# Optimization experiments

Hardware: AMD Instinct MI355X
Metric: run time of the kernel (lower is better)

The kernel has to match this reference:

```python
import jax, jax.numpy as jnp
import numpy as np

H = 16
D_MODEL = 1024
D_K = D_MODEL // H


def setup_inputs() -> dict:
    key = jax.random.key(0)
    ks = jax.random.split(key, 11)
    B, S = 4, 2048
    scale = 1.0 / np.sqrt(D_MODEL)
    inp = {
        "query": jax.random.normal(ks[0], (B, S, D_MODEL), dtype=jnp.float32),
        "key": jax.random.normal(ks[1], (B, S, D_MODEL), dtype=jnp.float32),
        "value": jax.random.normal(ks[2], (B, S, D_MODEL), dtype=jnp.float32),
        "Wq": jax.random.normal(ks[3], (D_MODEL, D_MODEL), dtype=jnp.float32) * scale,
        "bq": jnp.zeros((D_MODEL,), dtype=jnp.float32),
        "Wk": jax.random.normal(ks[4], (D_MODEL, D_MODEL), dtype=jnp.float32) * scale,
        "bk": jnp.zeros((D_MODEL,), dtype=jnp.float32),
        "Wv": jax.random.normal(ks[5], (D_MODEL, D_MODEL), dtype=jnp.float32) * scale,
        "bv": jnp.zeros((D_MODEL,), dtype=jnp.float32),
        "Wo": jax.random.normal(ks[6], (D_MODEL, D_MODEL), dtype=jnp.float32) * scale,
        "bo": jnp.zeros((D_MODEL,), dtype=jnp.float32),
    }
    return inp


def reference(query, key, value, Wq, bq, Wk, bk, Wv, bv, Wo, bo):
    B, S, _ = query.shape

    def proj(x, W, b):
        # nn.Linear: x @ W.T + b, then split heads -> [B, H, S, D_K]
        y = jnp.einsum("bsd,ed->bse", x, W) + b
        return y.reshape(B, S, H, D_K).transpose(0, 2, 1, 3)

    q = proj(query, Wq, bq)
    k = proj(key, Wk, bk)
    v = proj(value, Wv, bv)

    scores = jnp.einsum("bhqd,bhkd->bhqk", q, k) / jnp.sqrt(jnp.float32(D_K))
    attn = jax.nn.softmax(scores, axis=-1)
    out = jnp.einsum("bhqk,bhkd->bhqd", attn, v)  # [B,H,S,D_K]
    out = out.transpose(0, 2, 1, 3).reshape(B, S, H * D_K)
    # final linear (dropout disabled in eval / deterministic reference)
    return jnp.einsum("bsd,ed->bse", out, Wo) + bo
```

## Files before the change

### kernel.cpp

```cpp
#include <hip/hip_runtime.h>
#include <stdint.h>

typedef __attribute__((ext_vector_type(8))) short short8;
typedef __attribute__((ext_vector_type(4))) float floatx4;

#define DEV __device__ __forceinline__

DEV unsigned short f2bf(float x) {
  unsigned u = __float_as_uint(x);
  u += 0x7fffu + ((u >> 16) & 1u);
  return (unsigned short)(u >> 16);
}

DEV unsigned pkbf(float hi, float lo) {
  return __builtin_amdgcn_perm(__float_as_uint(hi) + 0x8000u,
                               __float_as_uint(lo) + 0x8000u, 0x07060302u);
}

DEV unsigned cvtpk(float a, float b) {
  unsigned r;
  asm("v_cvt_pk_bf16_f32 %0, %1, %2" : "=v"(r) : "v"(a), "v"(b));
  return r;
}

DEV void load_lds16(const unsigned short* g, unsigned short* l) {
  __builtin_amdgcn_global_load_lds(
      (const __attribute__((address_space(1))) void*)g,
      (__attribute__((address_space(3))) void*)l, 16, 0, 0);
}

DEV void lds_fence() { asm volatile("" ::: "memory"); }

#define ASM_VMCNT(n) asm volatile("s_waitcnt vmcnt(" #n ")" ::: "memory")
DEV void sched_fence() { __builtin_amdgcn_sched_barrier(0); }

__global__ void cvt_all(const float* __restrict__ Wq, const float* __restrict__ Wk,
                        const float* __restrict__ Wv, const float* __restrict__ Wo,
                        const float* __restrict__ Xq, const float* __restrict__ Xk,
                        const float* __restrict__ Xv,
                        unsigned short* __restrict__ Wb, unsigned short* __restrict__ XqB,
                        unsigned short* __restrict__ XkB, unsigned short* __restrict__ XvB) {
  int bid = blockIdx.x;
  const float* src;
  unsigned short* dst;
  int off;
  if (bid < 4096) {
    int sel = bid >> 10;
    src = sel == 0 ? Wq : sel == 1 ? Wk : sel == 2 ? Wv : Wo;
    dst = Wb + (size_t)sel * 1048576;
    off = bid & 1023;
  } else {
    bid -= 4096;
    int sel = bid >> 13;
    src = sel == 0 ? Xq : sel == 1 ? Xk : Xv;
    dst = sel == 0 ? XqB : sel == 1 ? XkB : XvB;
    off = bid & 8191;
  }
  int i = (off * 256 + threadIdx.x) * 4;
  float4 v = *(const float4*)(src + i);
  uint2 o;
  o.x = pkbf(v.y, v.x);
  o.y = pkbf(v.w, v.z);
  *(uint2*)(dst + i) = o;
}

#define SCQ (0.125f * 1.44269504089f)
__global__ __launch_bounds__(256, 3) void qkv_gemm(
    const unsigned short* __restrict__ XqB, const unsigned short* __restrict__ XkB,
    const unsigned short* __restrict__ XvB,
    const unsigned short* __restrict__ Wb,
    const float* __restrict__ bq, const float* __restrict__ bk, const float* __restrict__ bv,
    unsigned short* __restrict__ Qp, unsigned short* __restrict__ Kp,
    unsigned short* __restrict__ VTp) {
  __shared__ alignas(16) unsigned short Xs[3][128 * 32];
  __shared__ alignas(16) unsigned short Ws[3][128 * 32];
  const int z = blockIdx.z;
  const unsigned short* X = z == 0 ? XqB : z == 1 ? XkB : XvB;
  const unsigned short* W = Wb + (size_t)z * 1048576;
  const float* bias = z == 0 ? bq : z == 1 ? bk : bv;

  const int tid = threadIdx.x;
  const int lane = tid & 63, wave = tid >> 6;
  const int lcol = lane & 15, quad = lane >> 4;
  const int n2 = blockIdx.x + 8 * blockIdx.y;
  const int xcd = n2 & 7, ii = n2 >> 3;
  const int wo = (ii >> 3) * 128;
  const int xo = (xcd * 8 + (ii & 7)) * 128;
  const int wm = (wave & 1) * 64;
  const int wn = (wave >> 1) * 64;

  floatx4 acc[4][4];
  for (int mi = 0; mi < 4; ++mi)
    for (int ni = 0; ni < 4; ++ni)
      for (int r = 0; r < 4; ++r) acc[mi][ni][r] = 0.f;

  auto stage = [&](int kt, int buf) {
    const int k0 = kt * 32;
    int c = tid;
    load_lds16(W + (size_t)(wo + (c >> 2)) * 1024 + k0 + (c & 3) * 8, Ws[buf] + c * 8);
    load_lds16(X + (size_t)(xo + (c >> 2)) * 1024 + k0 + (c & 3) * 8, Xs[buf] + c * 8);
    c = tid + 256;
    load_lds16(W + (size_t)(wo + (c >> 2)) * 1024 + k0 + (c & 3) * 8, Ws[buf] + c * 8);
    load_lds16(X + (size_t)(xo + (c >> 2)) * 1024 + k0 + (c & 3) * 8, Xs[buf] + c * 8);
  };

  stage(0, 0);
  stage(1, 1);
  int cur = 0;
  for (int kt = 0; kt < 32; ++kt) {
    sched_fence();
    ASM_VMCNT(4);
    __builtin_amdgcn_s_barrier();
    sched_fence();
    int nb = cur + 2; if (nb >= 3) nb -= 3;
    stage((kt + 2) & 31, nb);
    const unsigned short* Ab = (z < 2) ? Ws[cur] : Xs[cur];
    const unsigned short* Bb = (z < 2) ? Xs[cur] : Ws[cur];
    short8 af[4], bfr[4];
#pragma unroll
    for (int mi = 0; mi < 4; ++mi)
      af[mi] = *(const short8*)(Ab + (wm + mi * 16 + lcol) * 32 + quad * 8);
#pragma unroll
    for (int ni = 0; ni < 4; ++ni)
      bfr[ni] = *(const short8*)(Bb + (wn + ni * 16 + lcol) * 32 + quad * 8);
#pragma unroll
    for (int mi = 0; mi < 4; ++mi)
#pragma unroll
      for (int ni = 0; ni < 4; ++ni)
        acc[mi][ni] = __builtin_amdgcn_mfma_f32_16x16x32_bf16(af[mi], bfr[ni], acc[mi][ni], 0, 0, 0);
    cur = (cur == 2) ? 0 : cur + 1;
  }

  if (z < 2) {
    unsigned short* Out = z == 0 ? Qp : Kp;
    const float scl = z == 0 ? SCQ : 1.f;
#pragma unroll
    for (int mi = 0; mi < 4; ++mi) {
      int dbase = wo + wm + mi * 16 + quad * 4;
      float4 bv4 = *(const float4*)(bias + dbase);
      int h = dbase >> 6, dk = dbase & 63;
#pragma unroll
      for (int ni = 0; ni < 4; ++ni) {
        int sg = xo + wn + ni * 16 + lcol;
        int bb = sg >> 11, ss = sg & 2047;
        uint2 o;
        o.x = pkbf((acc[mi][ni][1] + bv4.y) * scl, (acc[mi][ni][0] + bv4.x) * scl);
        o.y = pkbf((acc[mi][ni][3] + bv4.w) * scl, (acc[mi][ni][2] + bv4.z) * scl);
        *(uint2*)(Out + ((size_t)(bb * 16 + h) * 2048 + ss) * 64 + dk) = o;
      }
    }
  } else {
#pragma unroll
    for (int ni = 0; ni < 4; ++ni) {
      int dg = wo + wn + ni * 16 + lcol;
      float bvx = bias[dg];
      int h = dg >> 6, dk = dg & 63;
#pragma unroll
      for (int mi = 0; mi < 4; ++mi) {
        int sbase = xo + wm + mi * 16 + quad * 4;
        int bb = sbase >> 11, ss = sbase & 2047;
        uint2 o;
        o.x = pkbf(acc[mi][ni][1] + bvx, acc[mi][ni][0] + bvx);
        o.y = pkbf(acc[mi][ni][3] + bvx, acc[mi][ni][2] + bvx);
        *(uint2*)(VTp + ((size_t)(bb * 16 + h) * 64 + dk) * 2048 + ss) = o;
      }
    }
  }
}

__global__ __launch_bounds__(256, 3) void gemm_o(
    const unsigned short* __restrict__ A, const unsigned short* __restrict__ Bw,
    const float* __restrict__ bias, float* __restrict__ Out) {
  __shared__ alignas(16) unsigned short Cs[3][128 * 32];
  __shared__ alignas(16) unsigned short Wos[3][128 * 32];
  const int tid = threadIdx.x;
  const int lane = tid & 63, wave = tid >> 6;
  const int lcol = lane & 15, quad = lane >> 4;
  const int n2 = blockIdx.x + 8 * blockIdx.y;
  const int xcd = n2 & 7, ii = n2 >> 3;
  const int co = (ii >> 3) * 128;
  const int so = (xcd * 8 + (ii & 7)) * 128;
  const int wm = (wave & 1) * 64;
  const int wn = (wave >> 1) * 64;

  floatx4 acc[4][4];
  for (int mi = 0; mi < 4; ++mi)
    for (int ni = 0; ni < 4; ++ni)
      for (int r = 0; r < 4; ++r) acc[mi][ni][r] = 0.f;

  auto stage = [&](int kt, int buf) {
    const int k0 = kt * 32;
    int c = tid;
    load_lds16(Bw + (size_t)(co + (c >> 2)) * 1024 + k0 + (c & 3) * 8, Wos[buf] + c * 8);
    load_lds16(A  + (size_t)(so + (c >> 2)) * 1024 + k0 + (c & 3) * 8, Cs[buf] + c * 8);
    c = tid + 256;
    load_lds16(Bw + (size_t)(co + (c >> 2)) * 1024 + k0 + (c & 3) * 8, Wos[buf] + c * 8);
    load_lds16(A  + (size_t)(so + (c >> 2)) * 1024 + k0 + (c & 3) * 8, Cs[buf] + c * 8);
  };

  stage(0, 0);
  stage(1, 1);
  int cur = 0;
  for (int kt = 0; kt < 32; ++kt) {
    sched_fence();
    ASM_VMCNT(4);
    __builtin_amdgcn_s_barrier();
    sched_fence();
    int nb = cur + 2; if (nb >= 3) nb -= 3;
    stage((kt + 2) & 31, nb);
    short8 af[4], bfr[4];
#pragma unroll
    for (int mi = 0; mi < 4; ++mi)
      af[mi] = *(const short8*)(Wos[cur] + (wm + mi * 16 + lcol) * 32 + quad * 8);
#pragma unroll
    for (int ni = 0; ni < 4; ++ni)
      bfr[ni] = *(const short8*)(Cs[cur] + (wn + ni * 16 + lcol) * 32 + quad * 8);
#pragma unroll
    for (int mi = 0; mi < 4; ++mi)
#pragma unroll
      for (int ni = 0; ni < 4; ++ni)
        acc[mi][ni] = __builtin_amdgcn_mfma_f32_16x16x32_bf16(af[mi], bfr[ni], acc[mi][ni], 0, 0, 0);
    cur = (cur == 2) ? 0 : cur + 1;
  }
#pragma unroll
  for (int mi = 0; mi < 4; ++mi) {
    int cb = co + wm + mi * 16 + quad * 4;
    float4 bv4 = *(const float4*)(bias + cb);
#pragma unroll
    for (int ni = 0; ni < 4; ++ni) {
      int sg = so + wn + ni * 16 + lcol;
      float4 o;
      o.x = acc[mi][ni][0] + bv4.x;
      o.y = acc[mi][ni][1] + bv4.y;
      o.z = acc[mi][ni][2] + bv4.z;
      o.w = acc[mi][ni][3] + bv4.w;
      *(float4*)(Out + (size_t)sg * 1024 + cb) = o;
    }
  }
}

__global__ __launch_bounds__(256, 4) void attn_kernel(
    const unsigned short* __restrict__ Qp, const unsigned short* __restrict__ Kp,
    const unsigned short* __restrict__ VTp, unsigned short* __restrict__ Ctx) {
  __shared__ alignas(16) unsigned short Ks[2][64 * 64];
  __shared__ alignas(16) unsigned short Vt[64 * 64];
  __shared__ alignas(16) unsigned short Ps[128 * 64];

  const int tid = threadIdx.x;
  const int lane = tid & 63, wave = tid >> 6;
  const int lcol = lane & 15, quad = lane >> 4;
  const int wq = wave * 32;
  const int n = blockIdx.x + 16 * (blockIdx.y + 16 * blockIdx.z);
  const int xcd = n & 7, ii = n >> 3;
  const int hb = xcd * 8 + (ii & 7);
  const int qt = ii >> 3;
  const size_t bh = (size_t)hb * 2048 * 64;
  const int b = hb >> 4;
  const unsigned short* Qb = Qp + bh + (size_t)qt * 128 * 64;
  const unsigned short* Kb = Kp + bh;
  const unsigned short* VTb = VTp + bh;

#pragma unroll
  for (int i = 0; i < 4; ++i) {
    int p = tid + i * 256;
    int row = p >> 3, pj = p & 7;
    load_lds16(Qb + row * 64 + ((pj ^ (row & 7)) * 8), Ps + p * 8);
  }
#pragma unroll
  for (int i = 0; i < 2; ++i) {
    int p = tid + i * 256;
    int kr = p >> 3, kj = p & 7;
    load_lds16(Kb + kr * 64 + ((kj ^ (kr & 7)) * 8), Ks[0] + p * 8);
  }
  __syncthreads();

  short8 qf[2][2];
#pragma unroll
  for (int ni = 0; ni < 2; ++ni)
#pragma unroll
    for (int ks = 0; ks < 2; ++ks) {
      int row = wq + ni * 16 + lcol;
      qf[ni][ks] = *(const short8*)(Ps + row * 64 + (((ks * 4 + quad) ^ (row & 7)) * 8));
    }

  short8 ones;
#pragma unroll
  for (int j = 0; j < 8; ++j) ones[j] = (short)0x3f80;

  float M[2] = {-1e30f, -1e30f};
  floatx4 Oacc[2][4];
  floatx4 OaccL[2];
  for (int mi = 0; mi < 2; ++mi) {
    for (int nd = 0; nd < 4; ++nd)
      for (int r = 0; r < 4; ++r) Oacc[mi][nd][r] = 0.f;
    for (int r = 0; r < 4; ++r) OaccL[mi][r] = 0.f;
  }

  for (int jt = 0; jt < 32; ++jt) {
    const int cur = jt & 1;
#pragma unroll
    for (int i = 0; i < 2; ++i) {
      int p = tid + i * 256;
      int vr = p >> 3, vj = p & 7;
      load_lds16(VTb + (size_t)vr * 2048 + jt * 64 + ((vj ^ (vr & 7)) * 8), Vt + p * 8);
    }
    const int jn = (jt + 1) & 31;
#pragma unroll
    for (int i = 0; i < 2; ++i) {
      int p = tid + i * 256;
      int kr = p >> 3, kj = p & 7;
      load_lds16(Kb + (size_t)jn * 4096 + kr * 64 + ((kj ^ (kr & 7)) * 8), Ks[cur ^ 1] + p * 8);
    }

    const unsigned short* Kc = Ks[cur];
    floatx4 sacc[4][2];
    for (int mi = 0; mi < 4; ++mi)
      for (int ni = 0; ni < 2; ++ni)
        for (int r = 0; r < 4; ++r) sacc[mi][ni][r] = 0.f;
#pragma unroll
    for (int mi = 0; mi < 4; ++mi) {
      int row = mi * 16 + lcol;
      int sw = (row & 7);
      short8 kf0 = *(const short8*)(Kc + row * 64 + ((quad ^ sw) * 8));
      short8 kf1 = *(const short8*)(Kc + row * 64 + (((4 + quad) ^ sw) * 8));
#pragma unroll
      for (int ni = 0; ni < 2; ++ni) {
        sacc[mi][ni] = __builtin_amdgcn_mfma_f32_16x16x32_bf16(kf0, qf[ni][0], sacc[mi][ni], 0, 0, 0);
        sacc[mi][ni] = __builtin_amdgcn_mfma_f32_16x16x32_bf16(kf1, qf[ni][1], sacc[mi][ni], 0, 0, 0);
      }
    }

    float lmax[2];
#pragma unroll
    for (int ni = 0; ni < 2; ++ni) {
      float a0 = fmaxf(fmaxf(sacc[0][ni][0], sacc[0][ni][1]), sacc[0][ni][2]);
      float a1 = fmaxf(fmaxf(sacc[0][ni][3], sacc[1][ni][0]), sacc[1][ni][1]);
      float a2 = fmaxf(fmaxf(sacc[1][ni][2], sacc[1][ni][3]), sacc[2][ni][0]);
      float a3 = fmaxf(fmaxf(sacc[2][ni][1], sacc[2][ni][2]), sacc[2][ni][3]);
      float a4 = fmaxf(fmaxf(sacc[3][ni][0], sacc[3][ni][1]), sacc[3][ni][2]);
      float b0 = fmaxf(fmaxf(a0, a1), a2);
      float b1 = fmaxf(fmaxf(a3, a4), sacc[3][ni][3]);
      lmax[ni] = fmaxf(b0, b1);
    }
    const int skip = __all((lmax[0] <= M[0] + 8.f) & (lmax[1] <= M[1] + 8.f));
    if (!skip) {
      float alpha[2];
#pragma unroll
      for (int ni = 0; ni < 2; ++ni) {
        float m = lmax[ni];
        m = fmaxf(m, __shfl_xor(m, 16));
        m = fmaxf(m, __shfl_xor(m, 32));
        float mnew = fmaxf(M[ni], m);
        alpha[ni] = exp2f(M[ni] - mnew);
        M[ni] = mnew;
      }
#pragma unroll
      for (int mi = 0; mi < 2; ++mi)
#pragma unroll
        for (int r = 0; r < 4; ++r) {
          float a = __shfl(alpha[mi], quad * 4 + r);
          floatx4 av = {a, a, a, a};
#pragma unroll
          for (int nd = 0; nd < 4; ++nd) Oacc[mi][nd] *= av;
          OaccL[mi][r] *= a;
        }
    }
#pragma unroll
    for (int ni = 0; ni < 2; ++ni) {
      floatx4 mv = {M[ni], M[ni], M[ni], M[ni]};
#pragma unroll
      for (int mi = 0; mi < 4; ++mi) {
        floatx4 t = sacc[mi][ni] - mv;
        sacc[mi][ni][0] = exp2f(t[0]);
        sacc[mi][ni][1] = exp2f(t[1]);
        sacc[mi][ni][2] = exp2f(t[2]);
        sacc[mi][ni][3] = exp2f(t[3]);
      }
    }

#pragma unroll
    for (int ni = 0; ni < 2; ++ni) {
      int q = wq + ni * 16 + lcol;
      int sw = q & 7;
#pragma unroll
      for (int mi = 0; mi < 4; ++mi) {
        uint2 pw;
        pw.x = cvtpk(sacc[mi][ni][0], sacc[mi][ni][1]);
        pw.y = cvtpk(sacc[mi][ni][2], sacc[mi][ni][3]);
        int j = 2 * mi + (quad >> 1);
        *(uint2*)(Ps + q * 64 + ((j ^ sw) * 8) + (quad & 1) * 4) = pw;
      }
    }
    lds_fence();

    sched_fence();
    ASM_VMCNT(2);
    __builtin_amdgcn_s_barrier();
    sched_fence();

#pragma unroll
    for (int kk = 0; kk < 2; ++kk) {
      short8 pf[2];
#pragma unroll
      for (int mi = 0; mi < 2; ++mi) {
        int q = wq + mi * 16 + lcol;
        pf[mi] = *(const short8*)(Ps + q * 64 + (((kk * 4 + quad) ^ (q & 7)) * 8));
      }
#pragma unroll
      for (int nd = 0; nd < 4; ++nd) {
        int d = nd * 16 + lcol;
        short8 vf = *(const short8*)(Vt + d * 64 + (((kk * 4 + quad) ^ (d & 7)) * 8));
#pragma unroll
        for (int mi = 0; mi < 2; ++mi)
          Oacc[mi][nd] = __builtin_amdgcn_mfma_f32_16x16x32_bf16(pf[mi], vf, Oacc[mi][nd], 0, 0, 0);
      }
#pragma unroll
      for (int mi = 0; mi < 2; ++mi)
        OaccL[mi] = __builtin_amdgcn_mfma_f32_16x16x32_bf16(pf[mi], ones, OaccL[mi], 0, 0, 0);
    }
    lds_fence();
    __syncthreads();
  }

#pragma unroll
  for (int mi = 0; mi < 2; ++mi)
#pragma unroll
    for (int r = 0; r < 4; ++r) {
      float li = 1.f / OaccL[mi][r];
      int q = wq + mi * 16 + quad * 4 + r;
      int sw = q & 7;
#pragma unroll
      for (int nd = 0; nd < 4; ++nd) {
        int j = 2 * nd + (lcol >> 3);
        Ps[q * 64 + ((j ^ sw) * 8) + (lcol & 7)] = f2bf(Oacc[mi][nd][r] * li);
      }
    }
  __syncthreads();
#pragma unroll
  for (int i = 0; i < 4; ++i) {
    int c = tid + i * 256;
    int row = c >> 3, pj = c & 7;
    uint4 v = *(const uint4*)(Ps + row * 64 + ((pj ^ (row & 7)) * 8));
    *(uint4*)(Ctx + ((size_t)(b * 2048 + qt * 128 + row)) * 1024 + (hb & 15) * 64 + pj * 8) = v;
  }
}

extern "C" void kernel_launch(void* const* d_in, const int* in_sizes, int n_in,
                              void* d_out, int out_size, void* d_ws, size_t ws_size,
                              hipStream_t stream) {
  const float* query = (const float*)d_in[0];
  const float* key_  = (const float*)d_in[1];
  const float* value = (const float*)d_in[2];
  const float* Wq = (const float*)d_in[3];
  const float* bq = (const float*)d_in[4];
  const float* Wk = (const float*)d_in[5];
  const float* bk = (const float*)d_in[6];
  const float* Wv = (const float*)d_in[7];
  const float* bv = (const float*)d_in[8];
  const float* Wo = (const float*)d_in[9];
  const float* bo = (const float*)d_in[10];

  char* w = (char*)d_ws;
  unsigned short* Wb  = (unsigned short*)w; w += (size_t)4 * 1024 * 1024 * 2;
  unsigned short* Qp  = (unsigned short*)w; w += (size_t)8192 * 1024 * 2;
  unsigned short* Kp  = (unsigned short*)w; w += (size_t)8192 * 1024 * 2;
  unsigned short* VTp = (unsigned short*)w; w += (size_t)8192 * 1024 * 2;
  unsigned short* Ctx = (unsigned short*)w; w += (size_t)8192 * 1024 * 2;

  unsigned short* XqB = (unsigned short*)d_out;
  unsigned short* XkB = (unsigned short*)d_out + (size_t)8192 * 1024;
  unsigned short* XvB = Ctx;

  cvt_all<<<28672, 256, 0, stream>>>(Wq, Wk, Wv, Wo, query, key_, value,
                                     Wb, XqB, XkB, XvB);

  qkv_gemm<<<dim3(8, 64, 3), 256, 0, stream>>>(XqB, XkB, XvB, Wb,
                                               bq, bk, bv, Qp, Kp, VTp);

  attn_kernel<<<dim3(16, 16, 4), 256, 0, stream>>>(Qp, Kp, VTp, Ctx);

  gemm_o<<<dim3(8, 64), 256, 0, stream>>>(Ctx, Wb + (size_t)3 * 1048576, bo, (float*)d_out);
}
```

Measured before the change: 374.9 us.

## Rewrite attention with 32x32 MFMA, register-resident P, and triple-buffered K/V

The attention kernel moves from 16x16x32 to 32x32x16 bf16 MFMA tiles. Q is loaded straight from global into registers. P is kept in registers and shuffled into operand layout with v_permlane32_swap, so the LDS round-trip for P and one barrier per iteration go away. K and V tiles are now triple-buffered and prefetched two tiles ahead, and launch bounds drop from 4 to 3 blocks per SM to make room for the larger accumulators and buffers. The aim is less LDS traffic and sync overhead per KV tile, at the cost of more registers and more LDS per block, which lowers occupancy.

```diff
diff --git a/kernel.cpp b/kernel.cpp
--- a/kernel.cpp
+++ b/kernel.cpp
@@ -3,6 +3,7 @@
 
 typedef __attribute__((ext_vector_type(8))) short short8;
 typedef __attribute__((ext_vector_type(4))) float floatx4;
+typedef __attribute__((ext_vector_type(16))) float floatx16;
 
 #define DEV __device__ __forceinline__
 
@@ -21,6 +22,12 @@
   unsigned r;
   asm("v_cvt_pk_bf16_f32 %0, %1, %2" : "=v"(r) : "v"(a), "v"(b));
   return r;
+}
+
+DEV short8 pack4(unsigned a0, unsigned a1, unsigned b0, unsigned b1) {
+  union { unsigned u[4]; short8 s; } t;
+  t.u[0] = a0; t.u[1] = a1; t.u[2] = b0; t.u[3] = b1;
+  return t.s;
 }
 
 DEV void load_lds16(const unsigned short* g, unsigned short* l) {
@@ -239,16 +246,15 @@
   }
 }
 
-__global__ __launch_bounds__(256, 4) void attn_kernel(
+__global__ __launch_bounds__(256, 3) void attn_kernel(
     const unsigned short* __restrict__ Qp, const unsigned short* __restrict__ Kp,
     const unsigned short* __restrict__ VTp, unsigned short* __restrict__ Ctx) {
-  __shared__ alignas(16) unsigned short Ks[2][64 * 64];
-  __shared__ alignas(16) unsigned short Vt[64 * 64];
-  __shared__ alignas(16) unsigned short Ps[128 * 64];
+  __shared__ alignas(16) unsigned short Ks[3][64 * 64];
+  __shared__ alignas(16) unsigned short Vt[3][64 * 64];
 
   const int tid = threadIdx.x;
   const int lane = tid & 63, wave = tid >> 6;
-  const int lcol = lane & 15, quad = lane >> 4;
+  const int l31 = lane & 31, hh = lane >> 5;
   const int wq = wave * 32;
   const int n = blockIdx.x + 16 * (blockIdx.y + 16 * blockIdx.z);
   const int xcd = n & 7, ii = n >> 3;
@@ -260,187 +266,143 @@
   const unsigned short* Kb = Kp + bh;
   const unsigned short* VTb = VTp + bh;
 
-#pragma unroll
-  for (int i = 0; i < 4; ++i) {
-    int p = tid + i * 256;
-    int row = p >> 3, pj = p & 7;
-    load_lds16(Qb + row * 64 + ((pj ^ (row & 7)) * 8), Ps + p * 8);
-  }
-#pragma unroll
-  for (int i = 0; i < 2; ++i) {
-    int p = tid + i * 256;
-    int kr = p >> 3, kj = p & 7;
-    load_lds16(Kb + kr * 64 + ((kj ^ (kr & 7)) * 8), Ks[0] + p * 8);
-  }
-  __syncthreads();
-
-  short8 qf[2][2];
-#pragma unroll
-  for (int ni = 0; ni < 2; ++ni)
-#pragma unroll
-    for (int ks = 0; ks < 2; ++ks) {
-      int row = wq + ni * 16 + lcol;
-      qf[ni][ks] = *(const short8*)(Ps + row * 64 + (((ks * 4 + quad) ^ (row & 7)) * 8));
-    }
-
-  short8 ones;
-#pragma unroll
-  for (int j = 0; j < 8; ++j) ones[j] = (short)0x3f80;
-
-  float M[2] = {-1e30f, -1e30f};
-  floatx4 Oacc[2][4];
-  floatx4 OaccL[2];
-  for (int mi = 0; mi < 2; ++mi) {
-    for (int nd = 0; nd < 4; ++nd)
-      for (int r = 0; r < 4; ++r) Oacc[mi][nd][r] = 0.f;
-    for (int r = 0; r < 4; ++r) OaccL[mi][r] = 0.f;
-  }
-
-  for (int jt = 0; jt < 32; ++jt) {
-    const int cur = jt & 1;
+  short8 qf[4];
+#pragma unroll
+  for (int st = 0; st < 4; ++st)
+    qf[st] = *(const short8*)(Qb + (wq + l31) * 64 + st * 16 + hh * 8);
+
+  auto stageK = [&](int jt, int buf) {
+#pragma unroll
+    for (int i = 0; i < 2; ++i) {
+      int p = tid + i * 256;
+      int kr = p >> 3, kj = p & 7;
+      load_lds16(Kb + (size_t)jt * 4096 + kr * 64 + ((kj ^ (kr & 7)) * 8), Ks[buf] + p * 8);
+    }
+  };
+  auto stageV = [&](int jt, int buf) {
 #pragma unroll
     for (int i = 0; i < 2; ++i) {
       int p = tid + i * 256;
       int vr = p >> 3, vj = p & 7;
-      load_lds16(VTb + (size_t)vr * 2048 + jt * 64 + ((vj ^ (vr & 7)) * 8), Vt + p * 8);
-    }
-    const int jn = (jt + 1) & 31;
-#pragma unroll
-    for (int i = 0; i < 2; ++i) {
-      int p = tid + i * 256;
-      int kr = p >> 3, kj = p & 7;
-      load_lds16(Kb + (size_t)jn * 4096 + kr * 64 + ((kj ^ (kr & 7)) * 8), Ks[cur ^ 1] + p * 8);
-    }
+      load_lds16(VTb + (size_t)vr * 2048 + jt * 64 + ((vj ^ (vr & 7)) * 8), Vt[buf] + p * 8);
+    }
+  };
+
+  stageK(0, 0); stageV(0, 0);
+  stageK(1, 1); stageV(1, 1);
+  __syncthreads();
+
+  short8 ones;
+#pragma unroll
+  for (int j = 0; j < 8; ++j) ones[j] = (short)0x3f80;
+
+  float M = -1e30f;
+  floatx16 Oacc[2], OaccL;
+#pragma unroll
+  for (int r = 0; r < 16; ++r) { Oacc[0][r] = 0.f; Oacc[1][r] = 0.f; OaccL[r] = 0.f; }
+
+  int cur = 0;
+  for (int jt = 0; jt < 32; ++jt) {
+    int nb = cur + 2; if (nb >= 3) nb -= 3;
+    const int jn = (jt + 2) & 31;
+    stageK(jn, nb);
+    stageV(jn, nb);
 
     const unsigned short* Kc = Ks[cur];
-    floatx4 sacc[4][2];
-    for (int mi = 0; mi < 4; ++mi)
-      for (int ni = 0; ni < 2; ++ni)
-        for (int r = 0; r < 4; ++r) sacc[mi][ni][r] = 0.f;
-#pragma unroll
-    for (int mi = 0; mi < 4; ++mi) {
-      int row = mi * 16 + lcol;
-      int sw = (row & 7);
-      short8 kf0 = *(const short8*)(Kc + row * 64 + ((quad ^ sw) * 8));
-      short8 kf1 = *(const short8*)(Kc + row * 64 + (((4 + quad) ^ sw) * 8));
-#pragma unroll
-      for (int ni = 0; ni < 2; ++ni) {
-        sacc[mi][ni] = __builtin_amdgcn_mfma_f32_16x16x32_bf16(kf0, qf[ni][0], sacc[mi][ni], 0, 0, 0);
-        sacc[mi][ni] = __builtin_amdgcn_mfma_f32_16x16x32_bf16(kf1, qf[ni][1], sacc[mi][ni], 0, 0, 0);
-      }
-    }
-
-    float lmax[2];
-#pragma unroll
-    for (int ni = 0; ni < 2; ++ni) {
-      float a0 = fmaxf(fmaxf(sacc[0][ni][0], sacc[0][ni][1]), sacc[0][ni][2]);
-      float a1 = fmaxf(fmaxf(sacc[0][ni][3], sacc[1][ni][0]), sacc[1][ni][1]);
-      float a2 = fmaxf(fmaxf(sacc[1][ni][2], sacc[1][ni][3]), sacc[2][ni][0]);
-      float a3 = fmaxf(fmaxf(sacc[2][ni][1], sacc[2][ni][2]), sacc[2][ni][3]);
-      float a4 = fmaxf(fmaxf(sacc[3][ni][0], sacc[3][ni][1]), sacc[3][ni][2]);
-      float b0 = fmaxf(fmaxf(a0, a1), a2);
-      float b1 = fmaxf(fmaxf(a3, a4), sacc[3][ni][3]);
-      lmax[ni] = fmaxf(b0, b1);
-    }
-    const int skip = __all((lmax[0] <= M[0] + 8.f) & (lmax[1] <= M[1] + 8.f));
+    floatx16 sacc[2];
+#pragma unroll
+    for (int r = 0; r < 16; ++r) { sacc[0][r] = 0.f; sacc[1][r] = 0.f; }
+#pragma unroll
+    for (int st = 0; st < 4; ++st)
+#pragma unroll
+      for (int mk = 0; mk < 2; ++mk) {
+        int row = mk * 32 + l31;
+        short8 kf = *(const short8*)(Kc + row * 64 + (((2 * st + hh) ^ (row & 7)) * 8));
+        sacc[mk] = __builtin_amdgcn_mfma_f32_32x32x16_bf16(kf, qf[st], sacc[mk], 0, 0, 0);
+      }
+
+    float t8[8];
+#pragma unroll
+    for (int r = 0; r < 8; ++r)
+      t8[r] = fmaxf(fmaxf(sacc[0][r], sacc[0][r + 8]), fmaxf(sacc[1][r], sacc[1][r + 8]));
+    float t4a = fmaxf(t8[0], t8[4]), t4b = fmaxf(t8[1], t8[5]);
+    float t4c = fmaxf(t8[2], t8[6]), t4d = fmaxf(t8[3], t8[7]);
+    float mloc = fmaxf(fmaxf(t4a, t4b), fmaxf(t4c, t4d));
+    float m2 = fmaxf(mloc, __shfl_xor(mloc, 32));
+
+    const int skip = __all(m2 <= M + 8.f);
     if (!skip) {
-      float alpha[2];
-#pragma unroll
-      for (int ni = 0; ni < 2; ++ni) {
-        float m = lmax[ni];
-        m = fmaxf(m, __shfl_xor(m, 16));
-        m = fmaxf(m, __shfl_xor(m, 32));
-        float mnew = fmaxf(M[ni], m);
-        alpha[ni] = exp2f(M[ni] - mnew);
-        M[ni] = mnew;
-      }
-#pragma unroll
-      for (int mi = 0; mi < 2; ++mi)
-#pragma unroll
-        for (int r = 0; r < 4; ++r) {
-          float a = __shfl(alpha[mi], quad * 4 + r);
-          floatx4 av = {a, a, a, a};
-#pragma unroll
-          for (int nd = 0; nd < 4; ++nd) Oacc[mi][nd] *= av;
-          OaccL[mi][r] *= a;
-        }
-    }
-#pragma unroll
-    for (int ni = 0; ni < 2; ++ni) {
-      floatx4 mv = {M[ni], M[ni], M[ni], M[ni]};
-#pragma unroll
-      for (int mi = 0; mi < 4; ++mi) {
-        floatx4 t = sacc[mi][ni] - mv;
-        sacc[mi][ni][0] = exp2f(t[0]);
-        sacc[mi][ni][1] = exp2f(t[1]);
-        sacc[mi][ni][2] = exp2f(t[2]);
-        sacc[mi][ni][3] = exp2f(t[3]);
-      }
-    }
-
-#pragma unroll
-    for (int ni = 0; ni < 2; ++ni) {
-      int q = wq + ni * 16 + lcol;
-      int sw = q & 7;
-#pragma unroll
-      for (int mi = 0; mi < 4; ++mi) {
-        uint2 pw;
-        pw.x = cvtpk(sacc[mi][ni][0], sacc[mi][ni][1]);
-        pw.y = cvtpk(sacc[mi][ni][2], sacc[mi][ni][3]);
-        int j = 2 * mi + (quad >> 1);
-        *(uint2*)(Ps + q * 64 + ((j ^ sw) * 8) + (quad & 1) * 4) = pw;
-      }
-    }
-    lds_fence();
-
-    sched_fence();
-    ASM_VMCNT(2);
+      float mnew = fmaxf(M, m2);
+      float alpha = exp2f(M - mnew);
+      M = mnew;
+#pragma unroll
+      for (int r = 0; r < 16; ++r) {
+        int srcl = (r & 3) + 8 * (r >> 2) + hh * 4;
+        float ar = __shfl(alpha, srcl);
+        Oacc[0][r] *= ar;
+        Oacc[1][r] *= ar;
+        OaccL[r] *= ar;
+      }
+    }
+#pragma unroll
+    for (int mk = 0; mk < 2; ++mk)
+#pragma unroll
+      for (int r = 0; r < 16; ++r) sacc[mk][r] = exp2f(sacc[mk][r] - M);
+
+    unsigned wpk[2][4][2];
+#pragma unroll
+    for (int mk = 0; mk < 2; ++mk)
+#pragma unroll
+      for (int c = 0; c < 4; ++c) {
+        wpk[mk][c][0] = cvtpk(sacc[mk][4 * c + 0], sacc[mk][4 * c + 1]);
+        wpk[mk][c][1] = cvtpk(sacc[mk][4 * c + 2], sacc[mk][4 * c + 3]);
+      }
+
+    const unsigned short* Vc = Vt[cur];
+#pragma unroll
+    for (int kk = 0; kk < 4; ++kk) {
+      const int e = kk & 1, mk = kk >> 1;
+      unsigned a0 = wpk[mk][2 * e][0], b0 = wpk[mk][2 * e + 1][0];
+      unsigned a1 = wpk[mk][2 * e][1], b1 = wpk[mk][2 * e + 1][1];
+      asm("v_permlane32_swap_b32 %0, %1" : "+v"(a0), "+v"(b0));
+      asm("v_permlane32_swap_b32 %0, %1" : "+v"(a1), "+v"(b1));
+      short8 pa = pack4(a0, a1, b0, b1);
+#pragma unroll
+      for (int nd = 0; nd < 2; ++nd) {
+        int row = nd * 32 + l31;
+        short8 vf = *(const short8*)(Vc + row * 64 + (((2 * kk + hh) ^ (row & 7)) * 8));
+        Oacc[nd] = __builtin_amdgcn_mfma_f32_32x32x16_bf16(pa, vf, Oacc[nd], 0, 0, 0);
+      }
+      OaccL = __builtin_amdgcn_mfma_f32_32x32x16_bf16(pa, ones, OaccL, 0, 0, 0);
+    }
+
+    sched_fence();
+    ASM_VMCNT(4);
     __builtin_amdgcn_s_barrier();
     sched_fence();
-
-#pragma unroll
-    for (int kk = 0; kk < 2; ++kk) {
-      short8 pf[2];
-#pragma unroll
-      for (int mi = 0; mi < 2; ++mi) {
-        int q = wq + mi * 16 + lcol;
-        pf[mi] = *(const short8*)(Ps + q * 64 + (((kk * 4 + quad) ^ (q & 7)) * 8));
-      }
-#pragma unroll
-      for (int nd = 0; nd < 4; ++nd) {
-        int d = nd * 16 + lcol;
-        short8 vf = *(const short8*)(Vt + d * 64 + (((kk * 4 + quad) ^ (d & 7)) * 8));
-#pragma unroll
-        for (int mi = 0; mi < 2; ++mi)
-          Oacc[mi][nd] = __builtin_amdgcn_mfma_f32_16x16x32_bf16(pf[mi], vf, Oacc[mi][nd], 0, 0, 0);
-      }
-#pragma unroll
-      for (int mi = 0; mi < 2; ++mi)
-        OaccL[mi] = __builtin_amdgcn_mfma_f32_16x16x32_bf16(pf[mi], ones, OaccL[mi], 0, 0, 0);
-    }
-    lds_fence();
-    __syncthreads();
-  }
-
-#pragma unroll
-  for (int mi = 0; mi < 2; ++mi)
-#pragma unroll
-    for (int r = 0; r < 4; ++r) {
-      float li = 1.f / OaccL[mi][r];
-      int q = wq + mi * 16 + quad * 4 + r;
-      int sw = q & 7;
-#pragma unroll
-      for (int nd = 0; nd < 4; ++nd) {
-        int j = 2 * nd + (lcol >> 3);
-        Ps[q * 64 + ((j ^ sw) * 8) + (lcol & 7)] = f2bf(Oacc[mi][nd][r] * li);
-      }
+    cur = (cur == 2) ? 0 : cur + 1;
+  }
+
+  ASM_VMCNT(0);
+  __syncthreads();
+  unsigned short* Obuf = &Ks[0][0];
+  float linv[16];
+#pragma unroll
+  for (int r = 0; r < 16; ++r) linv[r] = 1.f / OaccL[r];
+#pragma unroll
+  for (int nd = 0; nd < 2; ++nd)
+#pragma unroll
+    for (int r = 0; r < 16; ++r) {
+      int q = wq + (r & 3) + 8 * (r >> 2) + hh * 4;
+      int d = nd * 32 + l31;
+      Obuf[q * 64 + (((d >> 3) ^ (q & 7)) * 8) + (d & 7)] = f2bf(Oacc[nd][r] * linv[r]);
     }
   __syncthreads();
 #pragma unroll
   for (int i = 0; i < 4; ++i) {
     int c = tid + i * 256;
     int row = c >> 3, pj = c & 7;
-    uint4 v = *(const uint4*)(Ps + row * 64 + ((pj ^ (row & 7)) * 8));
+    uint4 v = *(const uint4*)(Obuf + row * 64 + ((pj ^ (row & 7)) * 8));
     *(uint4*)(Ctx + ((size_t)(b * 2048 + qt * 128 + row)) * 1024 + (hb & 15) * 64 + pj * 8) = v;
   }
 }
```

New measurement: 375.6 us. Within noise of the previous version (+0.2%).
